# Optimization experiments

Hardware: AMD Instinct MI355X
Metric: run time of the kernel (lower is better)

Reference implementation:

```python
import jax, jax.numpy as jnp
import numpy as np

N = 1024
N_FEAT = 512
HID = 256
N_KERNEL = 10
KERNEL_DIM = 10
MB_DIM = N_KERNEL * KERNEL_DIM  # 100
CAT = HID + N_KERNEL  # concat width per block
EPS = 1e-3  # keras LayerNormalization default epsilon
ALPHA = 0.3  # keras LeakyReLU default


def setup_inputs() -> dict:
    key = jax.random.key(0)
    ks = jax.random.split(key, 16)
    def w(k, shape, std=0.1):
        return (jax.random.normal(k, shape, dtype=jnp.float32) * std)
    return {
        "x": jax.random.normal(ks[0], (N, N_FEAT), dtype=jnp.float32),
        # block 0
        "W0": w(ks[1], (N_FEAT, HID)), "b0": jnp.zeros((HID,), jnp.float32),
        "Wd0": w(ks[2], (HID, MB_DIM)), "bd0": jnp.zeros((MB_DIM,), jnp.float32),
        "beta0": jnp.zeros((CAT,), jnp.float32),
        # block 1 (input width = HID + N_KERNEL)
        "W1": w(ks[3], (CAT, HID)), "b1": jnp.zeros((HID,), jnp.float32),
        "Wd1": w(ks[4], (HID, MB_DIM)), "bd1": jnp.zeros((MB_DIM,), jnp.float32),
        "beta1": jnp.zeros((CAT,), jnp.float32),
        # final critic head
        "Wf": w(ks[5], (CAT, 1)), "bf": jnp.zeros((1,), jnp.float32),
    }


def _batch_diversity(M):
    # M: [N, n_kernel*kernel_dim] -> [N, n_kernel]
    M = M.reshape(-1, N_KERNEL, KERNEL_DIM)
    # pairwise L1 distance over kernel_dim: [N, N, n_kernel]
    l1 = jnp.abs(M[:, None, :, :] - M[None, :, :, :]).sum(axis=3)
    return jnp.exp(-l1).sum(axis=0)  # [N, n_kernel]


def _layer_norm_center_only(h, beta):
    mu = h.mean(axis=-1, keepdims=True)
    var = h.var(axis=-1, keepdims=True)
    return (h - mu) * jax.lax.rsqrt(var + EPS) + beta


def _block(x, W, b, Wd, bd, beta):
    h = x @ W + b                       # [N, HID]
    div = _batch_diversity(h @ Wd + bd)  # [N, N_KERNEL]
    h = jnp.concatenate([h, div], axis=1)  # [N, CAT]
    h = _layer_norm_center_only(h, beta)   # dropout is identity at inference
    return jax.nn.leaky_relu(h, ALPHA)


def reference(x, W0, b0, Wd0, bd0, beta0, W1, b1, Wd1, bd1, beta1, Wf, bf):
    h = _block(x, W0, b0, Wd0, bd0, beta0)
    h = _block(h, W1, b1, Wd1, bd1, beta1)
    return h @ Wf + bf  # [N, 1] critic value (WGGP: no sigmoid)
```

## Files before the change

### kernel.cpp

```cpp
#include <hip/hip_runtime.h>

typedef __attribute__((ext_vector_type(8))) short short8;
typedef __attribute__((ext_vector_type(4))) float f32x4;

#define EPS   1e-3f
#define ALPHA 0.3f

#define MFMA(a, b, c) __builtin_amdgcn_mfma_f32_16x16x32_bf16((a), (b), (c), 0, 0, 0)

__device__ __forceinline__ unsigned short f2bf(float f) {
    unsigned u = __float_as_uint(f);
    unsigned r = u + 0x7FFFu + ((u >> 16) & 1u);
    return (unsigned short)(r >> 16);
}
__device__ __forceinline__ float lrelu(float v) { return v > 0.f ? v : ALPHA * v; }

__global__ __launch_bounds__(256) void prep_kernel(
    const float* __restrict__ W0, const float* __restrict__ Wd0,
    const float* __restrict__ W1, const float* __restrict__ Wd1,
    const float* __restrict__ b0, const float* __restrict__ bd0,
    const float* __restrict__ b1, const float* __restrict__ bd1,
    unsigned short* __restrict__ Wc0bT, unsigned short* __restrict__ Wc1bT,
    float* __restrict__ bcomb0, float* __restrict__ bcomb1)
{
    const int bid = blockIdx.x, t = threadIdx.x;
    if (bid < 202) {
        const int half = t >> 7, c = t & 127;
        const int base = bid * 4 + half * 2;
#pragma unroll
        for (int rr = 0; rr < 2; ++rr) {
            const int row = base + rr;
            if (row < 512) {
                float s = 0.f;
                if (c < 100) {
                    const float* wp = W0 + (size_t)row * 256;
                    const float* dp = Wd0 + c;
                    float s0 = 0.f, s1 = 0.f, s2 = 0.f, s3 = 0.f;
                    for (int k = 0; k < 256; k += 4) {
                        s0 += wp[k]     * dp[k * 100];
                        s1 += wp[k + 1] * dp[(k + 1) * 100];
                        s2 += wp[k + 2] * dp[(k + 2) * 100];
                        s3 += wp[k + 3] * dp[(k + 3) * 100];
                    }
                    s = (s0 + s1) + (s2 + s3);
                }
                Wc0bT[(size_t)c * 512 + row] = f2bf(s);
            } else {
                const int a = row - 512;
                float s = 0.f;
                if (c < 100 && a < 266) {
                    const float* wp = W1 + (size_t)a * 256;
                    const float* dp = Wd1 + c;
                    float s0 = 0.f, s1 = 0.f, s2 = 0.f, s3 = 0.f;
                    for (int k = 0; k < 256; k += 4) {
                        s0 += wp[k]     * dp[k * 100];
                        s1 += wp[k + 1] * dp[(k + 1) * 100];
                        s2 += wp[k + 2] * dp[(k + 2) * 100];
                        s3 += wp[k + 3] * dp[(k + 3) * 100];
                    }
                    s = (s0 + s1) + (s2 + s3);
                }
                Wc1bT[(size_t)c * 296 + a] = f2bf(s);
            }
        }
    } else {
        const float* bb = (bid == 202) ? b0 : b1;
        const float* Wd = (bid == 202) ? Wd0 : Wd1;
        const float* bd = (bid == 202) ? bd0 : bd1;
        float* o = (bid == 202) ? bcomb0 : bcomb1;
        if (t < 128) {
            float s = 0.f;
            if (t < 100) {
                s = bd[t];
                float s0 = 0.f, s1 = 0.f;
                for (int k = 0; k < 256; k += 2) {
                    s0 += bb[k] * Wd[k * 100 + t];
                    s1 += bb[k + 1] * Wd[(k + 1) * 100 + t];
                }
                s += s0 + s1;
            }
            o[t] = s;
        }
    }
}

__global__ __launch_bounds__(256) void hm0_mfma(
    const float* __restrict__ x, const float* __restrict__ W0,
    const unsigned short* __restrict__ Wc0bT,
    const float* __restrict__ b0, const float* __restrict__ bcomb0,
    float* __restrict__ h0, float* __restrict__ Mt0)
{
    __shared__ unsigned short At[32][520];
    __shared__ unsigned short Bt[32][520];

    const int t = threadIdx.x, xt = blockIdx.x, yt = blockIdx.y;

    {
        const int row = t >> 3, kc = t & 7;
        const float* xp = x + (size_t)(xt * 32 + row) * 512 + kc * 64;
#pragma unroll
        for (int i = 0; i < 8; ++i) {
            const float4 lo = ((const float4*)xp)[i * 2];
            const float4 hi = ((const float4*)xp)[i * 2 + 1];
            short8 p;
            p[0] = f2bf(lo.x); p[1] = f2bf(lo.y); p[2] = f2bf(lo.z); p[3] = f2bf(lo.w);
            p[4] = f2bf(hi.x); p[5] = f2bf(hi.y); p[6] = f2bf(hi.z); p[7] = f2bf(hi.w);
            *(short8*)&At[row][kc * 64 + i * 8] = p;
        }
    }
    if (yt < 8) {
        const int kc = t >> 5, n = t & 31, col0 = yt * 32;
        for (int kk = 0; kk < 64; kk += 2) {
            const int k = kc * 64 + kk;
            const float a = W0[(size_t)k * 256 + col0 + n];
            const float b = W0[(size_t)(k + 1) * 256 + col0 + n];
            const unsigned pk = (unsigned)f2bf(a) | ((unsigned)f2bf(b) << 16);
            *(unsigned*)&Bt[n][k] = pk;
        }
    } else {
        const int c = t >> 3, kc = t & 7;
        const unsigned short* bp = Wc0bT + (size_t)((yt - 8) * 32 + c) * 512 + kc * 64;
#pragma unroll
        for (int i = 0; i < 8; ++i)
            *(short8*)&Bt[c][kc * 64 + i * 8] = ((const short8*)bp)[i];
    }
    __syncthreads();

    const int lane = t & 63, w = t >> 6;
    const int wr = w >> 1, wn = w & 1, r = lane & 15, g = lane >> 4;
    const int lrA = wr * 16 + r, lrB = wn * 16 + r;
    f32x4 acc0 = {0.f, 0.f, 0.f, 0.f}, acc1 = {0.f, 0.f, 0.f, 0.f};
#pragma unroll
    for (int k0 = 0; k0 < 512; k0 += 64) {
        acc0 = MFMA(*(const short8*)&At[lrA][k0 + g * 8],
                    *(const short8*)&Bt[lrB][k0 + g * 8], acc0);
        acc1 = MFMA(*(const short8*)&At[lrA][k0 + 32 + g * 8],
                    *(const short8*)&Bt[lrB][k0 + 32 + g * 8], acc1);
    }
    const f32x4 acc = acc0 + acc1;
    const int orow0 = xt * 32 + wr * 16 + g * 4;

    if (yt < 8) {
        const int bcol = yt * 32 + wn * 16 + r;
        const float bv = b0[bcol];
#pragma unroll
        for (int i = 0; i < 4; ++i)
            h0[(size_t)(orow0 + i) * 256 + bcol] = acc[i] + bv;
    } else {
        const int c = (yt - 8) * 32 + wn * 16 + r;
        if (c < 100) {
            const int kq = c / 10, d = c - kq * 10;
            const float bv = bcomb0[c];
            float* dst = Mt0 + (size_t)kq * (1024 * 16) + (size_t)orow0 * 16 + d;
#pragma unroll
            for (int i = 0; i < 4; ++i) dst[i * 16] = acc[i] + bv;
        }
    }
}

__global__ __launch_bounds__(256) void hm1_mfma(
    const unsigned short* __restrict__ a0b, const float* __restrict__ W1,
    const unsigned short* __restrict__ Wc1bT,
    const float* __restrict__ b1, const float* __restrict__ bcomb1,
    float* __restrict__ h1, float* __restrict__ Mt1)
{
    __shared__ unsigned short At[32][296];
    __shared__ unsigned short Bt[32][296];

    const int t = threadIdx.x, xt = blockIdx.x, yt = blockIdx.y;

    {
        const int row = t >> 3, kc = t & 7;
        const unsigned short* ap = a0b + (size_t)(xt * 32 + row) * 296;
        for (int i = kc; i < 37; i += 8)
            *(short8*)&At[row][i * 8] = ((const short8*)ap)[i];
    }
    if (yt < 8) {
        const int kc = t >> 5, n = t & 31, col0 = yt * 32;
        const int kkEnd = (kc == 7) ? 44 : 36;
        for (int kk = 0; kk < kkEnd; kk += 2) {
            const int k = kc * 36 + kk;
            const float a = (k < 266)     ? W1[(size_t)k * 256 + col0 + n] : 0.f;
            const float b = (k + 1 < 266) ? W1[(size_t)(k + 1) * 256 + col0 + n] : 0.f;
            const unsigned pk = (unsigned)f2bf(a) | ((unsigned)f2bf(b) << 16);
            *(unsigned*)&Bt[n][k] = pk;
        }
    } else {
        const int c = t >> 3, kc = t & 7;
        const unsigned short* bp = Wc1bT + (size_t)((yt - 8) * 32 + c) * 296;
        for (int i = kc; i < 37; i += 8)
            *(short8*)&Bt[c][i * 8] = ((const short8*)bp)[i];
    }
    __syncthreads();

    const int lane = t & 63, w = t >> 6;
    const int wr = w >> 1, wn = w & 1, r = lane & 15, g = lane >> 4;
    const int lrA = wr * 16 + r, lrB = wn * 16 + r;
    f32x4 acc0 = {0.f, 0.f, 0.f, 0.f}, acc1 = {0.f, 0.f, 0.f, 0.f};
#pragma unroll
    for (int k0 = 0; k0 < 256; k0 += 64) {
        acc0 = MFMA(*(const short8*)&At[lrA][k0 + g * 8],
                    *(const short8*)&Bt[lrB][k0 + g * 8], acc0);
        acc1 = MFMA(*(const short8*)&At[lrA][k0 + 32 + g * 8],
                    *(const short8*)&Bt[lrB][k0 + 32 + g * 8], acc1);
    }
    acc0 = MFMA(*(const short8*)&At[lrA][256 + g * 8],
                *(const short8*)&Bt[lrB][256 + g * 8], acc0);
    const f32x4 acc = acc0 + acc1;
    const int orow0 = xt * 32 + wr * 16 + g * 4;

    if (yt < 8) {
        const int bcol = yt * 32 + wn * 16 + r;
        const float bv = b1[bcol];
#pragma unroll
        for (int i = 0; i < 4; ++i)
            h1[(size_t)(orow0 + i) * 256 + bcol] = acc[i] + bv;
    } else {
        const int c = (yt - 8) * 32 + wn * 16 + r;
        if (c < 100) {
            const int kq = c / 10, d = c - kq * 10;
            const float bv = bcomb1[c];
            float* dst = Mt1 + (size_t)kq * (1024 * 16) + (size_t)orow0 * 16 + d;
#pragma unroll
            for (int i = 0; i < 4; ++i) dst[i * 16] = acc[i] + bv;
        }
    }
}

__global__ __launch_bounds__(256) void diversity_kernel(
    const float* __restrict__ Mt, float* __restrict__ divOut)
{
    __shared__ float Ms[1024 * 16];
    __shared__ float red[256];

    const int t = threadIdx.x;
    const float* src = Mt + (size_t)blockIdx.y * (1024 * 16);
    for (int i = t; i < 1024 * 4; i += 256)
        ((float4*)Ms)[i] = ((const float4*)src)[i];
    __syncthreads();

    const int il = t & 31, jc = t >> 5;
    const int i = blockIdx.x * 32 + il;

    const float4 m0 = *(const float4*)&Ms[i * 16];
    const float4 m1 = *(const float4*)&Ms[i * 16 + 4];
    const float4 m2 = *(const float4*)&Ms[i * 16 + 8];

    float acc = 0.f;
    const int jB = jc * 128;
#pragma unroll 2
    for (int j = jB; j < jB + 128; ++j) {
        const float4 v0 = *(const float4*)&Ms[j * 16];
        const float4 v1 = *(const float4*)&Ms[j * 16 + 4];
        const float4 v2 = *(const float4*)&Ms[j * 16 + 8];
        float l1 = fabsf(m0.x - v0.x) + fabsf(m0.y - v0.y)
                 + fabsf(m0.z - v0.z) + fabsf(m0.w - v0.w)
                 + fabsf(m1.x - v1.x) + fabsf(m1.y - v1.y)
                 + fabsf(m1.z - v1.z) + fabsf(m1.w - v1.w)
                 + fabsf(m2.x - v2.x) + fabsf(m2.y - v2.y);
        acc += __expf(-l1);
    }

    red[t] = acc;
    __syncthreads();
    if (t < 32) {
        float s = 0.f;
#pragma unroll
        for (int c = 0; c < 8; ++c) s += red[c * 32 + t];
        divOut[(size_t)(blockIdx.x * 32 + t) * 10 + blockIdx.y] = s;
    }
}

__global__ __launch_bounds__(256) void ln0_kernel(
    const float* __restrict__ h0, const float* __restrict__ div0,
    const float* __restrict__ beta0, unsigned short* __restrict__ a0b)
{
    const int t = threadIdx.x, lane = t & 63;
    const int row = blockIdx.x * 4 + (t >> 6);

    const float4 hv = ((const float4*)(h0 + (size_t)row * 256))[lane];
    const float dv = (lane < 10) ? div0[(size_t)row * 10 + lane] : 0.f;

    float s = hv.x + hv.y + hv.z + hv.w + dv;
    float q = hv.x * hv.x + hv.y * hv.y + hv.z * hv.z + hv.w * hv.w + dv * dv;
#pragma unroll
    for (int m = 32; m > 0; m >>= 1) { s += __shfl_xor(s, m); q += __shfl_xor(q, m); }

    const float mean = s * (1.f / 266.f);
    const float var  = q * (1.f / 266.f) - mean * mean;
    const float inv  = rsqrtf(var + EPS);

    const float4 bv = ((const float4*)beta0)[lane];
    ushort4 o;
    o.x = f2bf(lrelu((hv.x - mean) * inv + bv.x));
    o.y = f2bf(lrelu((hv.y - mean) * inv + bv.y));
    o.z = f2bf(lrelu((hv.z - mean) * inv + bv.z));
    o.w = f2bf(lrelu((hv.w - mean) * inv + bv.w));
    *(ushort4*)&a0b[(size_t)row * 296 + lane * 4] = o;

    if (lane < 10)
        a0b[(size_t)row * 296 + 256 + lane] = f2bf(lrelu((dv - mean) * inv + beta0[256 + lane]));
    else if (lane >= 16 && lane < 46)
        a0b[(size_t)row * 296 + 250 + lane] = 0;
}

__global__ __launch_bounds__(256) void ln_final(
    const float* __restrict__ h1, const float* __restrict__ div1,
    const float* __restrict__ beta1, const float* __restrict__ Wf,
    const float* __restrict__ bf, float* __restrict__ out)
{
    const int t = threadIdx.x, lane = t & 63;
    const int row = blockIdx.x * 4 + (t >> 6);

    const float4 hv = ((const float4*)(h1 + (size_t)row * 256))[lane];
    const float dv = (lane < 10) ? div1[(size_t)row * 10 + lane] : 0.f;

    float s = hv.x + hv.y + hv.z + hv.w + dv;
    float q = hv.x * hv.x + hv.y * hv.y + hv.z * hv.z + hv.w * hv.w + dv * dv;
#pragma unroll
    for (int m = 32; m > 0; m >>= 1) { s += __shfl_xor(s, m); q += __shfl_xor(q, m); }

    const float mean = s * (1.f / 266.f);
    const float var  = q * (1.f / 266.f) - mean * mean;
    const float inv  = rsqrtf(var + EPS);

    const float4 bv = ((const float4*)beta1)[lane];
    const float4 wf = ((const float4*)Wf)[lane];
    float d = lrelu((hv.x - mean) * inv + bv.x) * wf.x
            + lrelu((hv.y - mean) * inv + bv.y) * wf.y
            + lrelu((hv.z - mean) * inv + bv.z) * wf.z
            + lrelu((hv.w - mean) * inv + bv.w) * wf.w;
    if (lane < 10)
        d += lrelu((dv - mean) * inv + beta1[256 + lane]) * Wf[256 + lane];
#pragma unroll
    for (int m = 32; m > 0; m >>= 1) d += __shfl_xor(d, m);
    if (lane == 0) out[row] = d + bf[0];
}

extern "C" void kernel_launch(void* const* d_in, const int* in_sizes, int n_in,
                              void* d_out, int out_size, void* d_ws, size_t ws_size,
                              hipStream_t stream)
{
    const float* x     = (const float*)d_in[0];
    const float* W0    = (const float*)d_in[1];
    const float* b0    = (const float*)d_in[2];
    const float* Wd0   = (const float*)d_in[3];
    const float* bd0   = (const float*)d_in[4];
    const float* beta0 = (const float*)d_in[5];
    const float* W1    = (const float*)d_in[6];
    const float* b1    = (const float*)d_in[7];
    const float* Wd1   = (const float*)d_in[8];
    const float* bd1   = (const float*)d_in[9];
    const float* beta1 = (const float*)d_in[10];
    const float* Wf    = (const float*)d_in[11];
    const float* bf    = (const float*)d_in[12];
    float* out = (float*)d_out;

    float* fws = (float*)d_ws;
    float* h0     = fws;
    float* h1     = h0 + 1024 * 256;
    float* Mt0    = h1 + 1024 * 256;
    float* Mt1    = Mt0 + 10 * 1024 * 16;
    float* div0   = Mt1 + 10 * 1024 * 16;
    float* div1   = div0 + 1024 * 10;
    float* bcomb0 = div1 + 1024 * 10;
    float* bcomb1 = bcomb0 + 128;
    unsigned short* Wc0bT = (unsigned short*)(bcomb1 + 128);
    unsigned short* Wc1bT = Wc0bT + 128 * 512;
    unsigned short* a0b   = Wc1bT + 128 * 296;

    dim3 blk(256);

    prep_kernel<<<dim3(204), blk, 0, stream>>>(
        W0, Wd0, W1, Wd1, b0, bd0, b1, bd1, Wc0bT, Wc1bT, bcomb0, bcomb1);

    hm0_mfma<<<dim3(32, 12), blk, 0, stream>>>(
        x, W0, Wc0bT, b0, bcomb0, h0, Mt0);

    diversity_kernel<<<dim3(32, 10), blk, 0, stream>>>(Mt0, div0);

    ln0_kernel<<<dim3(256), blk, 0, stream>>>(h0, div0, beta0, a0b);

    hm1_mfma<<<dim3(32, 12), blk, 0, stream>>>(
        a0b, W1, Wc1bT, b1, bcomb1, h1, Mt1);

    diversity_kernel<<<dim3(32, 10), blk, 0, stream>>>(Mt1, div1);

    ln_final<<<dim3(256), blk, 0, stream>>>(h1, div1, beta1, Wf, bf, out);
}
```

Before: 75.99 us.

## Fuse weight prep, LayerNorm and diversity projection into per-row-tile stage kernels

Removes the prep kernel that pre-multiplied W·Wd and the separate LN0 kernel. Each 32-row block now computes the full h tile by looping over column tiles with double-buffered W staging, keeps h in shared memory as bf16, and then runs a second small MFMA against Wd to produce M. This cuts the launch count from 7 to 5 and removes intermediate global traffic. In exchange the grid shrinks from 384 blocks to 32, with large shared-memory use (about 114 KB), which leaves most CUs idle. The M path also changes numerics slightly because h is rounded to bf16 before the Wd product.

```diff
diff --git a/kernel.cpp b/kernel.cpp
--- a/kernel.cpp
+++ b/kernel.cpp
@@ -15,85 +15,73 @@
 }
 __device__ __forceinline__ float lrelu(float v) { return v > 0.f ? v : ALPHA * v; }
 
-__global__ __launch_bounds__(256) void prep_kernel(
-    const float* __restrict__ W0, const float* __restrict__ Wd0,
-    const float* __restrict__ W1, const float* __restrict__ Wd1,
-    const float* __restrict__ b0, const float* __restrict__ bd0,
-    const float* __restrict__ b1, const float* __restrict__ bd1,
-    unsigned short* __restrict__ Wc0bT, unsigned short* __restrict__ Wc1bT,
-    float* __restrict__ bcomb0, float* __restrict__ bcomb1)
-{
-    const int bid = blockIdx.x, t = threadIdx.x;
-    if (bid < 202) {
-        const int half = t >> 7, c = t & 127;
-        const int base = bid * 4 + half * 2;
-#pragma unroll
-        for (int rr = 0; rr < 2; ++rr) {
-            const int row = base + rr;
-            if (row < 512) {
-                float s = 0.f;
-                if (c < 100) {
-                    const float* wp = W0 + (size_t)row * 256;
-                    const float* dp = Wd0 + c;
-                    float s0 = 0.f, s1 = 0.f, s2 = 0.f, s3 = 0.f;
-                    for (int k = 0; k < 256; k += 4) {
-                        s0 += wp[k]     * dp[k * 100];
-                        s1 += wp[k + 1] * dp[(k + 1) * 100];
-                        s2 += wp[k + 2] * dp[(k + 2) * 100];
-                        s3 += wp[k + 3] * dp[(k + 3) * 100];
-                    }
-                    s = (s0 + s1) + (s2 + s3);
-                }
-                Wc0bT[(size_t)c * 512 + row] = f2bf(s);
-            } else {
-                const int a = row - 512;
-                float s = 0.f;
-                if (c < 100 && a < 266) {
-                    const float* wp = W1 + (size_t)a * 256;
-                    const float* dp = Wd1 + c;
-                    float s0 = 0.f, s1 = 0.f, s2 = 0.f, s3 = 0.f;
-                    for (int k = 0; k < 256; k += 4) {
-                        s0 += wp[k]     * dp[k * 100];
-                        s1 += wp[k + 1] * dp[(k + 1) * 100];
-                        s2 += wp[k + 2] * dp[(k + 2) * 100];
-                        s3 += wp[k + 3] * dp[(k + 3) * 100];
-                    }
-                    s = (s0 + s1) + (s2 + s3);
-                }
-                Wc1bT[(size_t)c * 296 + a] = f2bf(s);
-            }
-        }
-    } else {
-        const float* bb = (bid == 202) ? b0 : b1;
-        const float* Wd = (bid == 202) ? Wd0 : Wd1;
-        const float* bd = (bid == 202) ? bd0 : bd1;
-        float* o = (bid == 202) ? bcomb0 : bcomb1;
-        if (t < 128) {
-            float s = 0.f;
-            if (t < 100) {
-                s = bd[t];
-                float s0 = 0.f, s1 = 0.f;
-                for (int k = 0; k < 256; k += 2) {
-                    s0 += bb[k] * Wd[k * 100 + t];
-                    s1 += bb[k + 1] * Wd[(k + 1) * 100 + t];
-                }
-                s += s0 + s1;
-            }
-            o[t] = s;
-        }
-    }
-}
-
-__global__ __launch_bounds__(256) void hm0_mfma(
+__device__ __forceinline__ void m_phase(
+    const unsigned short (*Hb)[264], unsigned short (*WdT)[264],
+    const float* __restrict__ Wd, const float* __restrict__ bd,
+    float* __restrict__ Mt, int xt, int t)
+{
+#pragma unroll 4
+    for (int idx = t; idx < 112 * 256; idx += 256) {
+        const int c = idx % 112;
+        const int k = idx / 112;
+        WdT[c][k] = (c < 100) ? f2bf(Wd[k * 100 + c]) : (unsigned short)0;
+    }
+    __syncthreads();
+
+    const int lane = t & 63, w = t >> 6, r = lane & 15, g = lane >> 4;
+    for (int tile = w; tile < 14; tile += 4) {
+        const int rt = tile / 7, c7 = tile % 7;
+        const unsigned short* Ap = &Hb[rt * 16 + r][g * 8];
+        const unsigned short* Bp = &WdT[c7 * 16 + r][g * 8];
+        f32x4 a0 = {0.f, 0.f, 0.f, 0.f}, a1 = {0.f, 0.f, 0.f, 0.f};
+#pragma unroll
+        for (int k0 = 0; k0 < 256; k0 += 64) {
+            a0 = MFMA(*(const short8*)(Ap + k0),      *(const short8*)(Bp + k0),      a0);
+            a1 = MFMA(*(const short8*)(Ap + k0 + 32), *(const short8*)(Bp + k0 + 32), a1);
+        }
+        const f32x4 acc = a0 + a1;
+        const int c = c7 * 16 + r;
+        if (c < 100) {
+            const int kq = c / 10, d = c - kq * 10;
+            const float bv = bd[c];
+            float* dst = Mt + (size_t)kq * (1024 * 16)
+                       + (size_t)(xt * 32 + rt * 16 + g * 4) * 16 + d;
+#pragma unroll
+            for (int i = 0; i < 4; ++i) dst[(size_t)i * 16] = acc[i] + bv;
+        }
+    }
+}
+
+__global__ __launch_bounds__(256) void stage0_kernel(
     const float* __restrict__ x, const float* __restrict__ W0,
-    const unsigned short* __restrict__ Wc0bT,
-    const float* __restrict__ b0, const float* __restrict__ bcomb0,
+    const float* __restrict__ b0, const float* __restrict__ Wd0,
+    const float* __restrict__ bd0,
     float* __restrict__ h0, float* __restrict__ Mt0)
 {
-    __shared__ unsigned short At[32][520];
-    __shared__ unsigned short Bt[32][520];
-
-    const int t = threadIdx.x, xt = blockIdx.x, yt = blockIdx.y;
+    __shared__ __align__(16) char smem[116736];
+    unsigned short (*At)[520]  = (unsigned short(*)[520])(smem);
+    unsigned short (*BtA)[520] = (unsigned short(*)[520])(smem + 33280);
+    unsigned short (*BtB)[520] = (unsigned short(*)[520])(smem + 66560);
+    unsigned short (*Hb)[264]  = (unsigned short(*)[264])(smem + 99840);
+    unsigned short (*WdT)[264] = (unsigned short(*)[264])(smem + 33280);
+
+    const int t = threadIdx.x, xt = blockIdx.x;
+    const int lane = t & 63, w = t >> 6;
+
+    auto stageB = [&](int ct, unsigned short (*B)[520]) {
+        const int kr = t >> 3, nf = t & 7;
+#pragma unroll
+        for (int rnd = 0; rnd < 16; ++rnd) {
+            const int k = kr + rnd * 32;
+            const float4 v = *(const float4*)&W0[(size_t)k * 256 + ct * 32 + nf * 4];
+            B[nf * 4 + 0][k] = f2bf(v.x);
+            B[nf * 4 + 1][k] = f2bf(v.y);
+            B[nf * 4 + 2][k] = f2bf(v.z);
+            B[nf * 4 + 3][k] = f2bf(v.w);
+        }
+    };
+
+    stageB(0, BtA);
 
     {
         const int row = t >> 3, kc = t & 7;
@@ -108,123 +96,126 @@
             *(short8*)&At[row][kc * 64 + i * 8] = p;
         }
     }
-    if (yt < 8) {
-        const int kc = t >> 5, n = t & 31, col0 = yt * 32;
-        for (int kk = 0; kk < 64; kk += 2) {
-            const int k = kc * 64 + kk;
-            const float a = W0[(size_t)k * 256 + col0 + n];
-            const float b = W0[(size_t)(k + 1) * 256 + col0 + n];
-            const unsigned pk = (unsigned)f2bf(a) | ((unsigned)f2bf(b) << 16);
-            *(unsigned*)&Bt[n][k] = pk;
-        }
-    } else {
-        const int c = t >> 3, kc = t & 7;
-        const unsigned short* bp = Wc0bT + (size_t)((yt - 8) * 32 + c) * 512 + kc * 64;
-#pragma unroll
-        for (int i = 0; i < 8; ++i)
-            *(short8*)&Bt[c][kc * 64 + i * 8] = ((const short8*)bp)[i];
-    }
-    __syncthreads();
-
+    __syncthreads();
+
+    const int wr = w >> 1, wn = w & 1, r = lane & 15, g = lane >> 4;
+    for (int ct = 0; ct < 8; ++ct) {
+        unsigned short (*Bcur)[520] = (ct & 1) ? BtB : BtA;
+        if (ct < 7) stageB(ct + 1, (ct & 1) ? BtA : BtB);
+
+        const unsigned short* Ap = &At[wr * 16 + r][g * 8];
+        const unsigned short* Bp = &Bcur[wn * 16 + r][g * 8];
+        f32x4 a0 = {0.f, 0.f, 0.f, 0.f}, a1 = {0.f, 0.f, 0.f, 0.f};
+#pragma unroll
+        for (int k0 = 0; k0 < 512; k0 += 64) {
+            a0 = MFMA(*(const short8*)(Ap + k0),      *(const short8*)(Bp + k0),      a0);
+            a1 = MFMA(*(const short8*)(Ap + k0 + 32), *(const short8*)(Bp + k0 + 32), a1);
+        }
+        const f32x4 acc = a0 + a1;
+        const int bcol = ct * 32 + wn * 16 + r;
+        const float bv = b0[bcol];
+        const int orow = xt * 32 + wr * 16 + g * 4;
+        const int lrow = wr * 16 + g * 4;
+#pragma unroll
+        for (int i = 0; i < 4; ++i) {
+            const float hv = acc[i] + bv;
+            h0[(size_t)(orow + i) * 256 + bcol] = hv;
+            Hb[lrow + i][bcol] = f2bf(hv);
+        }
+        __syncthreads();
+    }
+
+    m_phase(Hb, WdT, Wd0, bd0, Mt0, xt, t);
+}
+
+__global__ __launch_bounds__(256) void stage1_kernel(
+    const float* __restrict__ h0, const float* __restrict__ div0,
+    const float* __restrict__ beta0,
+    const float* __restrict__ W1, const float* __restrict__ b1,
+    const float* __restrict__ Wd1, const float* __restrict__ bd1,
+    float* __restrict__ h1, float* __restrict__ Mt1)
+{
+    __shared__ __align__(16) char smem[94976];
+    unsigned short (*At)[296]  = (unsigned short(*)[296])(smem);
+    unsigned short (*Hb)[264]  = (unsigned short(*)[264])(smem + 18944);
+    unsigned short (*BtA)[296] = (unsigned short(*)[296])(smem + 35840);
+    unsigned short (*BtB)[296] = (unsigned short(*)[296])(smem + 54784);
+    unsigned short (*WdT)[264] = (unsigned short(*)[264])(smem + 35840);
+
+    const int t = threadIdx.x, xt = blockIdx.x;
     const int lane = t & 63, w = t >> 6;
+
+    auto stageB = [&](int ct, unsigned short (*B)[296]) {
+        const int kr = t >> 3, nf = t & 7;
+#pragma unroll
+        for (int rnd = 0; rnd < 9; ++rnd) {
+            const int k = kr + rnd * 32;
+            float4 v = make_float4(0.f, 0.f, 0.f, 0.f);
+            if (k < 266) v = *(const float4*)&W1[(size_t)k * 256 + ct * 32 + nf * 4];
+            B[nf * 4 + 0][k] = f2bf(v.x);
+            B[nf * 4 + 1][k] = f2bf(v.y);
+            B[nf * 4 + 2][k] = f2bf(v.z);
+            B[nf * 4 + 3][k] = f2bf(v.w);
+        }
+    };
+
+    stageB(0, BtA);
+
+    for (int rr = 0; rr < 8; ++rr) {
+        const int row = xt * 32 + w * 8 + rr;
+        const float4 hv = ((const float4*)(h0 + (size_t)row * 256))[lane];
+        const float dvv = (lane < 10) ? div0[(size_t)row * 10 + lane] : 0.f;
+        float s = hv.x + hv.y + hv.z + hv.w + dvv;
+        float q = hv.x * hv.x + hv.y * hv.y + hv.z * hv.z + hv.w * hv.w + dvv * dvv;
+#pragma unroll
+        for (int m = 32; m > 0; m >>= 1) { s += __shfl_xor(s, m); q += __shfl_xor(q, m); }
+        const float mean = s * (1.f / 266.f);
+        const float var  = q * (1.f / 266.f) - mean * mean;
+        const float inv  = rsqrtf(var + EPS);
+        const int lr = w * 8 + rr;
+        const float4 b4 = ((const float4*)beta0)[lane];
+        ushort4 o;
+        o.x = f2bf(lrelu((hv.x - mean) * inv + b4.x));
+        o.y = f2bf(lrelu((hv.y - mean) * inv + b4.y));
+        o.z = f2bf(lrelu((hv.z - mean) * inv + b4.z));
+        o.w = f2bf(lrelu((hv.w - mean) * inv + b4.w));
+        *(ushort4*)&At[lr][lane * 4] = o;
+        if (lane < 10)
+            At[lr][256 + lane] = f2bf(lrelu((dvv - mean) * inv + beta0[256 + lane]));
+        else if (lane < 40)
+            At[lr][256 + lane] = 0;
+    }
+    __syncthreads();
+
     const int wr = w >> 1, wn = w & 1, r = lane & 15, g = lane >> 4;
-    const int lrA = wr * 16 + r, lrB = wn * 16 + r;
-    f32x4 acc0 = {0.f, 0.f, 0.f, 0.f}, acc1 = {0.f, 0.f, 0.f, 0.f};
-#pragma unroll
-    for (int k0 = 0; k0 < 512; k0 += 64) {
-        acc0 = MFMA(*(const short8*)&At[lrA][k0 + g * 8],
-                    *(const short8*)&Bt[lrB][k0 + g * 8], acc0);
-        acc1 = MFMA(*(const short8*)&At[lrA][k0 + 32 + g * 8],
-                    *(const short8*)&Bt[lrB][k0 + 32 + g * 8], acc1);
-    }
-    const f32x4 acc = acc0 + acc1;
-    const int orow0 = xt * 32 + wr * 16 + g * 4;
-
-    if (yt < 8) {
-        const int bcol = yt * 32 + wn * 16 + r;
-        const float bv = b0[bcol];
-#pragma unroll
-        for (int i = 0; i < 4; ++i)
-            h0[(size_t)(orow0 + i) * 256 + bcol] = acc[i] + bv;
-    } else {
-        const int c = (yt - 8) * 32 + wn * 16 + r;
-        if (c < 100) {
-            const int kq = c / 10, d = c - kq * 10;
-            const float bv = bcomb0[c];
-            float* dst = Mt0 + (size_t)kq * (1024 * 16) + (size_t)orow0 * 16 + d;
-#pragma unroll
-            for (int i = 0; i < 4; ++i) dst[i * 16] = acc[i] + bv;
-        }
-    }
-}
-
-__global__ __launch_bounds__(256) void hm1_mfma(
-    const unsigned short* __restrict__ a0b, const float* __restrict__ W1,
-    const unsigned short* __restrict__ Wc1bT,
-    const float* __restrict__ b1, const float* __restrict__ bcomb1,
-    float* __restrict__ h1, float* __restrict__ Mt1)
-{
-    __shared__ unsigned short At[32][296];
-    __shared__ unsigned short Bt[32][296];
-
-    const int t = threadIdx.x, xt = blockIdx.x, yt = blockIdx.y;
-
-    {
-        const int row = t >> 3, kc = t & 7;
-        const unsigned short* ap = a0b + (size_t)(xt * 32 + row) * 296;
-        for (int i = kc; i < 37; i += 8)
-            *(short8*)&At[row][i * 8] = ((const short8*)ap)[i];
-    }
-    if (yt < 8) {
-        const int kc = t >> 5, n = t & 31, col0 = yt * 32;
-        const int kkEnd = (kc == 7) ? 44 : 36;
-        for (int kk = 0; kk < kkEnd; kk += 2) {
-            const int k = kc * 36 + kk;
-            const float a = (k < 266)     ? W1[(size_t)k * 256 + col0 + n] : 0.f;
-            const float b = (k + 1 < 266) ? W1[(size_t)(k + 1) * 256 + col0 + n] : 0.f;
-            const unsigned pk = (unsigned)f2bf(a) | ((unsigned)f2bf(b) << 16);
-            *(unsigned*)&Bt[n][k] = pk;
-        }
-    } else {
-        const int c = t >> 3, kc = t & 7;
-        const unsigned short* bp = Wc1bT + (size_t)((yt - 8) * 32 + c) * 296;
-        for (int i = kc; i < 37; i += 8)
-            *(short8*)&Bt[c][i * 8] = ((const short8*)bp)[i];
-    }
-    __syncthreads();
-
-    const int lane = t & 63, w = t >> 6;
-    const int wr = w >> 1, wn = w & 1, r = lane & 15, g = lane >> 4;
-    const int lrA = wr * 16 + r, lrB = wn * 16 + r;
-    f32x4 acc0 = {0.f, 0.f, 0.f, 0.f}, acc1 = {0.f, 0.f, 0.f, 0.f};
-#pragma unroll
-    for (int k0 = 0; k0 < 256; k0 += 64) {
-        acc0 = MFMA(*(const short8*)&At[lrA][k0 + g * 8],
-                    *(const short8*)&Bt[lrB][k0 + g * 8], acc0);
-        acc1 = MFMA(*(const short8*)&At[lrA][k0 + 32 + g * 8],
-                    *(const short8*)&Bt[lrB][k0 + 32 + g * 8], acc1);
-    }
-    acc0 = MFMA(*(const short8*)&At[lrA][256 + g * 8],
-                *(const short8*)&Bt[lrB][256 + g * 8], acc0);
-    const f32x4 acc = acc0 + acc1;
-    const int orow0 = xt * 32 + wr * 16 + g * 4;
-
-    if (yt < 8) {
-        const int bcol = yt * 32 + wn * 16 + r;
+    for (int ct = 0; ct < 8; ++ct) {
+        unsigned short (*Bcur)[296] = (ct & 1) ? BtB : BtA;
+        if (ct < 7) stageB(ct + 1, (ct & 1) ? BtA : BtB);
+
+        const unsigned short* Ap = &At[wr * 16 + r][g * 8];
+        const unsigned short* Bp = &Bcur[wn * 16 + r][g * 8];
+        f32x4 a0 = {0.f, 0.f, 0.f, 0.f}, a1 = {0.f, 0.f, 0.f, 0.f};
+#pragma unroll
+        for (int k0 = 0; k0 < 256; k0 += 64) {
+            a0 = MFMA(*(const short8*)(Ap + k0),      *(const short8*)(Bp + k0),      a0);
+            a1 = MFMA(*(const short8*)(Ap + k0 + 32), *(const short8*)(Bp + k0 + 32), a1);
+        }
+        a0 = MFMA(*(const short8*)(Ap + 256), *(const short8*)(Bp + 256), a0);
+        const f32x4 acc = a0 + a1;
+        const int bcol = ct * 32 + wn * 16 + r;
         const float bv = b1[bcol];
-#pragma unroll
-        for (int i = 0; i < 4; ++i)
-            h1[(size_t)(orow0 + i) * 256 + bcol] = acc[i] + bv;
-    } else {
-        const int c = (yt - 8) * 32 + wn * 16 + r;
-        if (c < 100) {
-            const int kq = c / 10, d = c - kq * 10;
-            const float bv = bcomb1[c];
-            float* dst = Mt1 + (size_t)kq * (1024 * 16) + (size_t)orow0 * 16 + d;
-#pragma unroll
-            for (int i = 0; i < 4; ++i) dst[i * 16] = acc[i] + bv;
-        }
-    }
+        const int orow = xt * 32 + wr * 16 + g * 4;
+        const int lrow = wr * 16 + g * 4;
+#pragma unroll
+        for (int i = 0; i < 4; ++i) {
+            const float hv = acc[i] + bv;
+            h1[(size_t)(orow + i) * 256 + bcol] = hv;
+            Hb[lrow + i][bcol] = f2bf(hv);
+        }
+        __syncthreads();
+    }
+
+    m_phase(Hb, WdT, Wd1, bd1, Mt1, xt, t);
 }
 
 __global__ __launch_bounds__(256) void diversity_kernel(
@@ -269,39 +260,6 @@
         for (int c = 0; c < 8; ++c) s += red[c * 32 + t];
         divOut[(size_t)(blockIdx.x * 32 + t) * 10 + blockIdx.y] = s;
     }
-}
-
-__global__ __launch_bounds__(256) void ln0_kernel(
-    const float* __restrict__ h0, const float* __restrict__ div0,
-    const float* __restrict__ beta0, unsigned short* __restrict__ a0b)
-{
-    const int t = threadIdx.x, lane = t & 63;
-    const int row = blockIdx.x * 4 + (t >> 6);
-
-    const float4 hv = ((const float4*)(h0 + (size_t)row * 256))[lane];
-    const float dv = (lane < 10) ? div0[(size_t)row * 10 + lane] : 0.f;
-
-    float s = hv.x + hv.y + hv.z + hv.w + dv;
-    float q = hv.x * hv.x + hv.y * hv.y + hv.z * hv.z + hv.w * hv.w + dv * dv;
-#pragma unroll
-    for (int m = 32; m > 0; m >>= 1) { s += __shfl_xor(s, m); q += __shfl_xor(q, m); }
-
-    const float mean = s * (1.f / 266.f);
-    const float var  = q * (1.f / 266.f) - mean * mean;
-    const float inv  = rsqrtf(var + EPS);
-
-    const float4 bv = ((const float4*)beta0)[lane];
-    ushort4 o;
-    o.x = f2bf(lrelu((hv.x - mean) * inv + bv.x));
-    o.y = f2bf(lrelu((hv.y - mean) * inv + bv.y));
-    o.z = f2bf(lrelu((hv.z - mean) * inv + bv.z));
-    o.w = f2bf(lrelu((hv.w - mean) * inv + bv.w));
-    *(ushort4*)&a0b[(size_t)row * 296 + lane * 4] = o;
-
-    if (lane < 10)
-        a0b[(size_t)row * 296 + 256 + lane] = f2bf(lrelu((dv - mean) * inv + beta0[256 + lane]));
-    else if (lane >= 16 && lane < 46)
-        a0b[(size_t)row * 296 + 250 + lane] = 0;
 }
 
 __global__ __launch_bounds__(256) void ln_final(
@@ -357,32 +315,21 @@
     float* out = (float*)d_out;
 
     float* fws = (float*)d_ws;
-    float* h0     = fws;
-    float* h1     = h0 + 1024 * 256;
-    float* Mt0    = h1 + 1024 * 256;
-    float* Mt1    = Mt0 + 10 * 1024 * 16;
-    float* div0   = Mt1 + 10 * 1024 * 16;
-    float* div1   = div0 + 1024 * 10;
-    float* bcomb0 = div1 + 1024 * 10;
-    float* bcomb1 = bcomb0 + 128;
-    unsigned short* Wc0bT = (unsigned short*)(bcomb1 + 128);
-    unsigned short* Wc1bT = Wc0bT + 128 * 512;
-    unsigned short* a0b   = Wc1bT + 128 * 296;
+    float* h0   = fws;
+    float* h1   = h0 + 1024 * 256;
+    float* Mt0  = h1 + 1024 * 256;
+    float* Mt1  = Mt0 + 10 * 1024 * 16;
+    float* div0 = Mt1 + 10 * 1024 * 16;
+    float* div1 = div0 + 1024 * 10;
 
     dim3 blk(256);
 
-    prep_kernel<<<dim3(204), blk, 0, stream>>>(
-        W0, Wd0, W1, Wd1, b0, bd0, b1, bd1, Wc0bT, Wc1bT, bcomb0, bcomb1);
-
-    hm0_mfma<<<dim3(32, 12), blk, 0, stream>>>(
-        x, W0, Wc0bT, b0, bcomb0, h0, Mt0);
+    stage0_kernel<<<dim3(32), blk, 0, stream>>>(x, W0, b0, Wd0, bd0, h0, Mt0);
 
     diversity_kernel<<<dim3(32, 10), blk, 0, stream>>>(Mt0, div0);
 
-    ln0_kernel<<<dim3(256), blk, 0, stream>>>(h0, div0, beta0, a0b);
-
-    hm1_mfma<<<dim3(32, 12), blk, 0, stream>>>(
-        a0b, W1, Wc1bT, b1, bcomb1, h1, Mt1);
+    stage1_kernel<<<dim3(32), blk, 0, stream>>>(
+        h0, div0, beta0, W1, b1, Wd1, bd1, h1, Mt1);
 
     diversity_kernel<<<dim3(32, 10), blk, 0, stream>>>(Mt1, div1);
 
```

Measured after the change: 118.0 us. +55.3%, slower.

## Fuse layernorm into diversity kernel via last-block counter; MFMA weight precompose

Applied to the files above, without the earlier changes.

The layernorm kernels are folded into the diversity kernel. An atomic counter per row tile lets the last of the 10 kernel-column blocks run the layernorm and leaky ReLU, or the final head, for that tile. This removes two launches and their round trips through memory. The prep kernel's scalar Wc = W·Wd products are replaced by a bf16 MFMA tiled GEMM with half the blocks, and the diversity loads shrink from float4 to float2. The counters are reset inside the preceding GEMM kernel, and the fused tail adds threadfence and atomic ordering requirements.

```diff
diff --git a/kernel.cpp b/kernel.cpp
--- a/kernel.cpp
+++ b/kernel.cpp
@@ -24,60 +24,86 @@
     float* __restrict__ bcomb0, float* __restrict__ bcomb1)
 {
     const int bid = blockIdx.x, t = threadIdx.x;
-    if (bid < 202) {
-        const int half = t >> 7, c = t & 127;
-        const int base = bid * 4 + half * 2;
-#pragma unroll
-        for (int rr = 0; rr < 2; ++rr) {
-            const int row = base + rr;
-            if (row < 512) {
-                float s = 0.f;
-                if (c < 100) {
-                    const float* wp = W0 + (size_t)row * 256;
-                    const float* dp = Wd0 + c;
-                    float s0 = 0.f, s1 = 0.f, s2 = 0.f, s3 = 0.f;
-                    for (int k = 0; k < 256; k += 4) {
-                        s0 += wp[k]     * dp[k * 100];
-                        s1 += wp[k + 1] * dp[(k + 1) * 100];
-                        s2 += wp[k + 2] * dp[(k + 2) * 100];
-                        s3 += wp[k + 3] * dp[(k + 3) * 100];
-                    }
-                    s = (s0 + s1) + (s2 + s3);
+    if (bid < 100) {
+        __shared__ unsigned short Ab[32][264];
+        __shared__ unsigned short BbT[32][264];
+        const float *Wsrc, *Wdsrc;
+        unsigned short* Cdst;
+        int ldc, ft, ct, arows;
+        if (bid < 64) { ft = bid & 15; ct = bid >> 4; Wsrc = W0; Wdsrc = Wd0;
+                        Cdst = Wc0bT; ldc = 512; arows = 512; }
+        else { const int s = bid - 64; ft = s % 9; ct = s / 9;
+               Wsrc = W1; Wdsrc = Wd1; Cdst = Wc1bT; ldc = 296; arows = 266; }
+
+        {
+            const int row = t >> 3, kc = t & 7;
+            const int f = ft * 32 + row;
+            if (f < arows) {
+                const float* wp = Wsrc + (size_t)f * 256 + kc * 32;
+#pragma unroll
+                for (int i = 0; i < 8; ++i) {
+                    const float4 v = ((const float4*)wp)[i];
+                    Ab[row][kc * 32 + i * 4 + 0] = f2bf(v.x);
+                    Ab[row][kc * 32 + i * 4 + 1] = f2bf(v.y);
+                    Ab[row][kc * 32 + i * 4 + 2] = f2bf(v.z);
+                    Ab[row][kc * 32 + i * 4 + 3] = f2bf(v.w);
                 }
-                Wc0bT[(size_t)c * 512 + row] = f2bf(s);
             } else {
-                const int a = row - 512;
-                float s = 0.f;
-                if (c < 100 && a < 266) {
-                    const float* wp = W1 + (size_t)a * 256;
-                    const float* dp = Wd1 + c;
-                    float s0 = 0.f, s1 = 0.f, s2 = 0.f, s3 = 0.f;
-                    for (int k = 0; k < 256; k += 4) {
-                        s0 += wp[k]     * dp[k * 100];
-                        s1 += wp[k + 1] * dp[(k + 1) * 100];
-                        s2 += wp[k + 2] * dp[(k + 2) * 100];
-                        s3 += wp[k + 3] * dp[(k + 3) * 100];
-                    }
-                    s = (s0 + s1) + (s2 + s3);
-                }
-                Wc1bT[(size_t)c * 296 + a] = f2bf(s);
+#pragma unroll
+                for (int i = 0; i < 8; ++i)
+                    *(ushort4*)&Ab[row][kc * 32 + i * 4] = make_ushort4(0, 0, 0, 0);
             }
         }
+        for (int idx = t; idx < 2048; idx += 256) {
+            const int h = idx >> 3, c4 = idx & 7;
+            const int cbase = ct * 32 + c4 * 4;
+            float v[4];
+            if (cbase + 3 < 100) {
+                const float4 q = *(const float4*)&Wdsrc[(size_t)h * 100 + cbase];
+                v[0] = q.x; v[1] = q.y; v[2] = q.z; v[3] = q.w;
+            } else {
+#pragma unroll
+                for (int j = 0; j < 4; ++j)
+                    v[j] = (cbase + j < 100) ? Wdsrc[(size_t)h * 100 + cbase + j] : 0.f;
+            }
+#pragma unroll
+            for (int j = 0; j < 4; ++j) BbT[c4 * 4 + j][h] = f2bf(v[j]);
+        }
+        __syncthreads();
+
+        const int lane = t & 63, w = t >> 6;
+        const int cr = w & 1, fr = w >> 1, r = lane & 15, g = lane >> 4;
+        const unsigned short* Ap = &BbT[cr * 16 + r][g * 8];
+        const unsigned short* Bp = &Ab[fr * 16 + r][g * 8];
+        f32x4 a0 = {0.f, 0.f, 0.f, 0.f}, a1 = {0.f, 0.f, 0.f, 0.f};
+#pragma unroll
+        for (int k0 = 0; k0 < 256; k0 += 64) {
+            a0 = MFMA(*(const short8*)(Ap + k0),      *(const short8*)(Bp + k0),      a0);
+            a1 = MFMA(*(const short8*)(Ap + k0 + 32), *(const short8*)(Bp + k0 + 32), a1);
+        }
+        const f32x4 acc = a0 + a1;
+        const int crow = ct * 32 + cr * 16 + g * 4;
+        const int fcol = ft * 32 + fr * 16 + r;
+#pragma unroll
+        for (int i = 0; i < 4; ++i)
+            Cdst[(size_t)(crow + i) * ldc + fcol] = f2bf(acc[i]);
     } else {
-        const float* bb = (bid == 202) ? b0 : b1;
-        const float* Wd = (bid == 202) ? Wd0 : Wd1;
-        const float* bd = (bid == 202) ? bd0 : bd1;
-        float* o = (bid == 202) ? bcomb0 : bcomb1;
+        const float* bb = (bid == 100) ? b0 : b1;
+        const float* Wd = (bid == 100) ? Wd0 : Wd1;
+        const float* bd = (bid == 100) ? bd0 : bd1;
+        float* o = (bid == 100) ? bcomb0 : bcomb1;
         if (t < 128) {
             float s = 0.f;
             if (t < 100) {
                 s = bd[t];
-                float s0 = 0.f, s1 = 0.f;
-                for (int k = 0; k < 256; k += 2) {
-                    s0 += bb[k] * Wd[k * 100 + t];
+                float s0 = 0.f, s1 = 0.f, s2 = 0.f, s3 = 0.f;
+                for (int k = 0; k < 256; k += 4) {
+                    s0 += bb[k]     * Wd[k * 100 + t];
                     s1 += bb[k + 1] * Wd[(k + 1) * 100 + t];
+                    s2 += bb[k + 2] * Wd[(k + 2) * 100 + t];
+                    s3 += bb[k + 3] * Wd[(k + 3) * 100 + t];
                 }
-                s += s0 + s1;
+                s += (s0 + s1) + (s2 + s3);
             }
             o[t] = s;
         }
@@ -88,12 +114,14 @@
     const float* __restrict__ x, const float* __restrict__ W0,
     const unsigned short* __restrict__ Wc0bT,
     const float* __restrict__ b0, const float* __restrict__ bcomb0,
-    float* __restrict__ h0, float* __restrict__ Mt0)
+    float* __restrict__ h0, float* __restrict__ Mt0, int* __restrict__ cnt0)
 {
     __shared__ unsigned short At[32][520];
     __shared__ unsigned short Bt[32][520];
 
     const int t = threadIdx.x, xt = blockIdx.x, yt = blockIdx.y;
+
+    if (xt == 0 && yt == 0 && t < 32) cnt0[t] = 0;
 
     {
         const int row = t >> 3, kc = t & 7;
@@ -129,15 +157,15 @@
     const int lane = t & 63, w = t >> 6;
     const int wr = w >> 1, wn = w & 1, r = lane & 15, g = lane >> 4;
     const int lrA = wr * 16 + r, lrB = wn * 16 + r;
-    f32x4 acc0 = {0.f, 0.f, 0.f, 0.f}, acc1 = {0.f, 0.f, 0.f, 0.f};
+    f32x4 a0 = {0.f, 0.f, 0.f, 0.f}, a1 = {0.f, 0.f, 0.f, 0.f};
 #pragma unroll
     for (int k0 = 0; k0 < 512; k0 += 64) {
-        acc0 = MFMA(*(const short8*)&At[lrA][k0 + g * 8],
-                    *(const short8*)&Bt[lrB][k0 + g * 8], acc0);
-        acc1 = MFMA(*(const short8*)&At[lrA][k0 + 32 + g * 8],
-                    *(const short8*)&Bt[lrB][k0 + 32 + g * 8], acc1);
-    }
-    const f32x4 acc = acc0 + acc1;
+        a0 = MFMA(*(const short8*)&At[lrA][k0 + g * 8],
+                  *(const short8*)&Bt[lrB][k0 + g * 8], a0);
+        a1 = MFMA(*(const short8*)&At[lrA][k0 + 32 + g * 8],
+                  *(const short8*)&Bt[lrB][k0 + 32 + g * 8], a1);
+    }
+    const f32x4 acc = a0 + a1;
     const int orow0 = xt * 32 + wr * 16 + g * 4;
 
     if (yt < 8) {
@@ -162,12 +190,14 @@
     const unsigned short* __restrict__ a0b, const float* __restrict__ W1,
     const unsigned short* __restrict__ Wc1bT,
     const float* __restrict__ b1, const float* __restrict__ bcomb1,
-    float* __restrict__ h1, float* __restrict__ Mt1)
+    float* __restrict__ h1, float* __restrict__ Mt1, int* __restrict__ cnt1)
 {
     __shared__ unsigned short At[32][296];
     __shared__ unsigned short Bt[32][296];
 
     const int t = threadIdx.x, xt = blockIdx.x, yt = blockIdx.y;
+
+    if (xt == 0 && yt == 0 && t < 32) cnt1[t] = 0;
 
     {
         const int row = t >> 3, kc = t & 7;
@@ -196,17 +226,17 @@
     const int lane = t & 63, w = t >> 6;
     const int wr = w >> 1, wn = w & 1, r = lane & 15, g = lane >> 4;
     const int lrA = wr * 16 + r, lrB = wn * 16 + r;
-    f32x4 acc0 = {0.f, 0.f, 0.f, 0.f}, acc1 = {0.f, 0.f, 0.f, 0.f};
+    f32x4 a0 = {0.f, 0.f, 0.f, 0.f}, a1 = {0.f, 0.f, 0.f, 0.f};
 #pragma unroll
     for (int k0 = 0; k0 < 256; k0 += 64) {
-        acc0 = MFMA(*(const short8*)&At[lrA][k0 + g * 8],
-                    *(const short8*)&Bt[lrB][k0 + g * 8], acc0);
-        acc1 = MFMA(*(const short8*)&At[lrA][k0 + 32 + g * 8],
-                    *(const short8*)&Bt[lrB][k0 + 32 + g * 8], acc1);
-    }
-    acc0 = MFMA(*(const short8*)&At[lrA][256 + g * 8],
-                *(const short8*)&Bt[lrB][256 + g * 8], acc0);
-    const f32x4 acc = acc0 + acc1;
+        a0 = MFMA(*(const short8*)&At[lrA][k0 + g * 8],
+                  *(const short8*)&Bt[lrB][k0 + g * 8], a0);
+        a1 = MFMA(*(const short8*)&At[lrA][k0 + 32 + g * 8],
+                  *(const short8*)&Bt[lrB][k0 + 32 + g * 8], a1);
+    }
+    a0 = MFMA(*(const short8*)&At[lrA][256 + g * 8],
+              *(const short8*)&Bt[lrB][256 + g * 8], a0);
+    const f32x4 acc = a0 + a1;
     const int orow0 = xt * 32 + wr * 16 + g * 4;
 
     if (yt < 8) {
@@ -227,24 +257,30 @@
     }
 }
 
-__global__ __launch_bounds__(256) void diversity_kernel(
-    const float* __restrict__ Mt, float* __restrict__ divOut)
+template<int TAIL>
+__global__ __launch_bounds__(256) void div_kernel(
+    const float* __restrict__ Mt, float* __restrict__ divOut,
+    const float* __restrict__ h, const float* __restrict__ beta,
+    const float* __restrict__ Wf, const float* __restrict__ bfv,
+    float* __restrict__ outF, unsigned short* __restrict__ outB,
+    int* __restrict__ cnt)
 {
     __shared__ float Ms[1024 * 16];
     __shared__ float red[256];
-
-    const int t = threadIdx.x;
-    const float* src = Mt + (size_t)blockIdx.y * (1024 * 16);
+    __shared__ int wsel;
+
+    const int t = threadIdx.x, rt = blockIdx.x, k = blockIdx.y;
+
+    const float* src = Mt + (size_t)k * (1024 * 16);
     for (int i = t; i < 1024 * 4; i += 256)
         ((float4*)Ms)[i] = ((const float4*)src)[i];
     __syncthreads();
 
     const int il = t & 31, jc = t >> 5;
-    const int i = blockIdx.x * 32 + il;
-
+    const int i = rt * 32 + il;
     const float4 m0 = *(const float4*)&Ms[i * 16];
     const float4 m1 = *(const float4*)&Ms[i * 16 + 4];
-    const float4 m2 = *(const float4*)&Ms[i * 16 + 8];
+    const float2 m2 = *(const float2*)&Ms[i * 16 + 8];
 
     float acc = 0.f;
     const int jB = jc * 128;
@@ -252,7 +288,7 @@
     for (int j = jB; j < jB + 128; ++j) {
         const float4 v0 = *(const float4*)&Ms[j * 16];
         const float4 v1 = *(const float4*)&Ms[j * 16 + 4];
-        const float4 v2 = *(const float4*)&Ms[j * 16 + 8];
+        const float2 v2 = *(const float2*)&Ms[j * 16 + 8];
         float l1 = fabsf(m0.x - v0.x) + fabsf(m0.y - v0.y)
                  + fabsf(m0.z - v0.z) + fabsf(m0.w - v0.w)
                  + fabsf(m1.x - v1.x) + fabsf(m1.y - v1.y)
@@ -267,74 +303,54 @@
         float s = 0.f;
 #pragma unroll
         for (int c = 0; c < 8; ++c) s += red[c * 32 + t];
-        divOut[(size_t)(blockIdx.x * 32 + t) * 10 + blockIdx.y] = s;
-    }
-}
-
-__global__ __launch_bounds__(256) void ln0_kernel(
-    const float* __restrict__ h0, const float* __restrict__ div0,
-    const float* __restrict__ beta0, unsigned short* __restrict__ a0b)
-{
-    const int t = threadIdx.x, lane = t & 63;
-    const int row = blockIdx.x * 4 + (t >> 6);
-
-    const float4 hv = ((const float4*)(h0 + (size_t)row * 256))[lane];
-    const float dv = (lane < 10) ? div0[(size_t)row * 10 + lane] : 0.f;
-
-    float s = hv.x + hv.y + hv.z + hv.w + dv;
-    float q = hv.x * hv.x + hv.y * hv.y + hv.z * hv.z + hv.w * hv.w + dv * dv;
-#pragma unroll
-    for (int m = 32; m > 0; m >>= 1) { s += __shfl_xor(s, m); q += __shfl_xor(q, m); }
-
-    const float mean = s * (1.f / 266.f);
-    const float var  = q * (1.f / 266.f) - mean * mean;
-    const float inv  = rsqrtf(var + EPS);
-
-    const float4 bv = ((const float4*)beta0)[lane];
-    ushort4 o;
-    o.x = f2bf(lrelu((hv.x - mean) * inv + bv.x));
-    o.y = f2bf(lrelu((hv.y - mean) * inv + bv.y));
-    o.z = f2bf(lrelu((hv.z - mean) * inv + bv.z));
-    o.w = f2bf(lrelu((hv.w - mean) * inv + bv.w));
-    *(ushort4*)&a0b[(size_t)row * 296 + lane * 4] = o;
-
-    if (lane < 10)
-        a0b[(size_t)row * 296 + 256 + lane] = f2bf(lrelu((dv - mean) * inv + beta0[256 + lane]));
-    else if (lane >= 16 && lane < 46)
-        a0b[(size_t)row * 296 + 250 + lane] = 0;
-}
-
-__global__ __launch_bounds__(256) void ln_final(
-    const float* __restrict__ h1, const float* __restrict__ div1,
-    const float* __restrict__ beta1, const float* __restrict__ Wf,
-    const float* __restrict__ bf, float* __restrict__ out)
-{
-    const int t = threadIdx.x, lane = t & 63;
-    const int row = blockIdx.x * 4 + (t >> 6);
-
-    const float4 hv = ((const float4*)(h1 + (size_t)row * 256))[lane];
-    const float dv = (lane < 10) ? div1[(size_t)row * 10 + lane] : 0.f;
-
-    float s = hv.x + hv.y + hv.z + hv.w + dv;
-    float q = hv.x * hv.x + hv.y * hv.y + hv.z * hv.z + hv.w * hv.w + dv * dv;
-#pragma unroll
-    for (int m = 32; m > 0; m >>= 1) { s += __shfl_xor(s, m); q += __shfl_xor(q, m); }
-
-    const float mean = s * (1.f / 266.f);
-    const float var  = q * (1.f / 266.f) - mean * mean;
-    const float inv  = rsqrtf(var + EPS);
-
-    const float4 bv = ((const float4*)beta1)[lane];
-    const float4 wf = ((const float4*)Wf)[lane];
-    float d = lrelu((hv.x - mean) * inv + bv.x) * wf.x
-            + lrelu((hv.y - mean) * inv + bv.y) * wf.y
-            + lrelu((hv.z - mean) * inv + bv.z) * wf.z
-            + lrelu((hv.w - mean) * inv + bv.w) * wf.w;
-    if (lane < 10)
-        d += lrelu((dv - mean) * inv + beta1[256 + lane]) * Wf[256 + lane];
-#pragma unroll
-    for (int m = 32; m > 0; m >>= 1) d += __shfl_xor(d, m);
-    if (lane == 0) out[row] = d + bf[0];
+        divOut[(size_t)(rt * 32 + t) * 10 + k] = s;
+    }
+
+    __threadfence();
+    __syncthreads();
+    if (t == 0) wsel = atomicAdd(&cnt[rt], 1);
+    __syncthreads();
+    if (wsel != 9) return;
+    __threadfence();
+
+    const int lane = t & 63, w = t >> 6;
+    for (int rr = 0; rr < 8; ++rr) {
+        const int row = rt * 32 + w * 8 + rr;
+        const float4 hv = ((const float4*)(h + (size_t)row * 256))[lane];
+        const float dv = (lane < 10) ? divOut[(size_t)row * 10 + lane] : 0.f;
+        float s = hv.x + hv.y + hv.z + hv.w + dv;
+        float q = hv.x * hv.x + hv.y * hv.y + hv.z * hv.z + hv.w * hv.w + dv * dv;
+#pragma unroll
+        for (int m = 32; m > 0; m >>= 1) { s += __shfl_xor(s, m); q += __shfl_xor(q, m); }
+        const float mean = s * (1.f / 266.f);
+        const float var  = q * (1.f / 266.f) - mean * mean;
+        const float inv  = rsqrtf(var + EPS);
+        const float4 b4 = ((const float4*)beta)[lane];
+        if constexpr (TAIL == 1) {
+            ushort4 o;
+            o.x = f2bf(lrelu((hv.x - mean) * inv + b4.x));
+            o.y = f2bf(lrelu((hv.y - mean) * inv + b4.y));
+            o.z = f2bf(lrelu((hv.z - mean) * inv + b4.z));
+            o.w = f2bf(lrelu((hv.w - mean) * inv + b4.w));
+            *(ushort4*)&outB[(size_t)row * 296 + lane * 4] = o;
+            if (lane < 10)
+                outB[(size_t)row * 296 + 256 + lane] =
+                    f2bf(lrelu((dv - mean) * inv + beta[256 + lane]));
+            else if (lane >= 16 && lane < 46)
+                outB[(size_t)row * 296 + 250 + lane] = 0;
+        } else {
+            const float4 wf = ((const float4*)Wf)[lane];
+            float d = lrelu((hv.x - mean) * inv + b4.x) * wf.x
+                    + lrelu((hv.y - mean) * inv + b4.y) * wf.y
+                    + lrelu((hv.z - mean) * inv + b4.z) * wf.z
+                    + lrelu((hv.w - mean) * inv + b4.w) * wf.w;
+            if (lane < 10)
+                d += lrelu((dv - mean) * inv + beta[256 + lane]) * Wf[256 + lane];
+#pragma unroll
+            for (int m = 32; m > 0; m >>= 1) d += __shfl_xor(d, m);
+            if (lane == 0) outF[row] = d + bfv[0];
+        }
+    }
 }
 
 extern "C" void kernel_launch(void* const* d_in, const int* in_sizes, int n_in,
@@ -365,26 +381,26 @@
     float* div1   = div0 + 1024 * 10;
     float* bcomb0 = div1 + 1024 * 10;
     float* bcomb1 = bcomb0 + 128;
-    unsigned short* Wc0bT = (unsigned short*)(bcomb1 + 128);
+    int*   cnt0   = (int*)(bcomb1 + 128);
+    int*   cnt1   = cnt0 + 32;
+    unsigned short* Wc0bT = (unsigned short*)(cnt1 + 32);
     unsigned short* Wc1bT = Wc0bT + 128 * 512;
     unsigned short* a0b   = Wc1bT + 128 * 296;
 
     dim3 blk(256);
 
-    prep_kernel<<<dim3(204), blk, 0, stream>>>(
+    prep_kernel<<<dim3(102), blk, 0, stream>>>(
         W0, Wd0, W1, Wd1, b0, bd0, b1, bd1, Wc0bT, Wc1bT, bcomb0, bcomb1);
 
     hm0_mfma<<<dim3(32, 12), blk, 0, stream>>>(
-        x, W0, Wc0bT, b0, bcomb0, h0, Mt0);
-
-    diversity_kernel<<<dim3(32, 10), blk, 0, stream>>>(Mt0, div0);
-
-    ln0_kernel<<<dim3(256), blk, 0, stream>>>(h0, div0, beta0, a0b);
+        x, W0, Wc0bT, b0, bcomb0, h0, Mt0, cnt0);
+
+    div_kernel<1><<<dim3(32, 10), blk, 0, stream>>>(
+        Mt0, div0, h0, beta0, nullptr, nullptr, nullptr, a0b, cnt0);
 
     hm1_mfma<<<dim3(32, 12), blk, 0, stream>>>(
-        a0b, W1, Wc1bT, b1, bcomb1, h1, Mt1);
-
-    diversity_kernel<<<dim3(32, 10), blk, 0, stream>>>(Mt1, div1);
-
-    ln_final<<<dim3(256), blk, 0, stream>>>(h1, div1, beta1, Wf, bf, out);
-}
+        a0b, W1, Wc1bT, b1, bcomb1, h1, Mt1, cnt1);
+
+    div_kernel<2><<<dim3(32, 10), blk, 0, stream>>>(
+        Mt1, div1, h1, beta1, Wf, bf, out, nullptr, cnt1);
+}
```

Result: slower. 115.9 us (+52.6%).
